# Kernel optimization log

Measured on AMD Instinct MI355X. Metric: run time of the kernel, lower is better.

## Reference

```python
import jax, jax.numpy as jnp
import numpy as np

N = 4096
D_IN = 1024
D_Q = 1024
D_V = 1024

def setup_inputs() -> dict:
    key = jax.random.key(0)
    ks = jax.random.split(key, 8)
    # x scaled down a bit so exp() of raw (unstable, no max-subtract) scores stays finite,
    # matching the original module's numerics regime.
    x = jax.random.normal(ks[0], (N, D_IN), dtype=jnp.float32) * 0.02
    mask = jax.random.uniform(ks[1], (N, N), dtype=jnp.float32)
    s = 1.0 / np.sqrt(D_IN)
    Wq = jax.random.normal(ks[2], (D_IN, D_Q), dtype=jnp.float32) * s
    bq = jax.random.normal(ks[3], (D_Q,), dtype=jnp.float32) * 0.02
    Wk = jax.random.normal(ks[4], (D_IN, D_Q), dtype=jnp.float32) * s
    bk = jax.random.normal(ks[5], (D_Q,), dtype=jnp.float32) * 0.02
    Wv = jax.random.normal(ks[6], (D_IN, D_V), dtype=jnp.float32) * s
    bv = jax.random.normal(ks[7], (D_V,), dtype=jnp.float32) * 0.02
    return {"x": x, "mask": mask, "Wq": Wq, "bq": bq, "Wk": Wk, "bk": bk, "Wv": Wv, "bv": bv}

def reference(x, mask, Wq, bq, Wk, bk, Wv, bv):
    # Q, K, V projections (nn.Linear: x @ W + b, here W stored as [in, out])
    Q = x @ Wq + bq          # [N, Dq]
    K = x @ Wk + bk          # [N, Dq]
    V = x @ Wv + bv          # [N, Dv]
    scale = 1.0              # default scale in original forward
    scores = scale * (Q @ K.T)   # [N, N]
    scores = mask * scores       # elementwise multiplicative mask
    # Faithful to original (quirky) normalization:
    # exp(S) / sum(exp(S), axis=1)[None, :]  -> row-sums broadcast across ROWS
    e = jnp.exp(scores)                       # [N, N]
    denom = jnp.sum(e, axis=1)[None, :]       # [1, N]
    softmax = e / denom                       # [N, N]
    return softmax @ V                        # [N, Dv]
```

## Files before the change

### kernel.cpp

```cpp
#include <hip/hip_runtime.h>
#include <hip/hip_bf16.h>


#define N_TOK 4096
#define D_DIM 1024
#define VS_SCALE 131072.0f

typedef __bf16 bf16x8 __attribute__((ext_vector_type(8)));
typedef __bf16 bf16x4 __attribute__((ext_vector_type(4)));
typedef float  f32x4  __attribute__((ext_vector_type(4)));

typedef const __attribute__((address_space(1))) char g_char;
typedef __attribute__((address_space(3))) char lds_char;

__device__ inline unsigned char f32_to_fp8(float f) {
    return (unsigned char)(__builtin_amdgcn_cvt_pk_fp8_f32(f, f, 0, false) & 0xff);
}

__global__ void cvt_and_bias(const float* __restrict__ x, __bf16* __restrict__ xb,
                             const float* __restrict__ bq, const float* __restrict__ bk,
                             const float* __restrict__ bv, float* __restrict__ bcat) {
    int b = blockIdx.x;
    if (b < 4096) {
        int i = (b * 256 + threadIdx.x) * 4;
        float4 v = *(const float4*)(x + i);
        bf16x4 o;
        o.x = (__bf16)v.x; o.y = (__bf16)v.y;
        o.z = (__bf16)v.z; o.w = (__bf16)v.w;
        *(bf16x4*)(xb + i) = o;
    } else {
        int i = (b - 4096) * 256 + threadIdx.x;
        if (i < 1024) bcat[i] = bq[i];
        else if (i < 2048) bcat[i] = bk[i - 1024];
        else if (i < 3072) bcat[i] = bv[i - 2048];
    }
}

__global__ void transpose_w3(const float* __restrict__ Wq, const float* __restrict__ Wk,
                             const float* __restrict__ Wv, __bf16* __restrict__ outT) {
    const float* in = (blockIdx.z == 0) ? Wq : (blockIdx.z == 1) ? Wk : Wv;
    __bf16* oT = outT + (size_t)blockIdx.z * 1024 * 1024;
    __shared__ float t[64][65];
    const int c0 = blockIdx.x * 64, r0 = blockIdx.y * 64;
    const int tid = threadIdx.x;
#pragma unroll
    for (int k = 0; k < 16; k++) {
        int lin = tid + k * 256;
        int r = lin >> 6, c = lin & 63;
        t[r][c] = in[(size_t)(r0 + r) * 1024 + c0 + c];
    }
    __syncthreads();
#pragma unroll
    for (int k = 0; k < 16; k++) {
        int lin = tid + k * 256;
        int c = lin >> 6, r = lin & 63;
        oT[(size_t)(c0 + c) * 1024 + r0 + r] = (__bf16)t[r][c];
    }
}

__global__ void scale_transpose(const __bf16* __restrict__ V, int ldv,
                                const float* __restrict__ denom,
                                unsigned char* __restrict__ VT8) {
    __shared__ float t[64][65];
    __shared__ float rd[64];
    const int d0 = blockIdx.x * 64, j0 = blockIdx.y * 64;
    const int tid = threadIdx.x;
    if (tid < 64) rd[tid] = VS_SCALE / denom[j0 + tid];
    __syncthreads();
#pragma unroll
    for (int k = 0; k < 16; k++) {
        int lin = tid + k * 256;
        int j = lin >> 6, d = lin & 63;
        t[j][d] = (float)V[(size_t)(j0 + j) * ldv + d0 + d] * rd[j];
    }
    __syncthreads();
#pragma unroll
    for (int k = 0; k < 16; k++) {
        int lin = tid + k * 256;
        int d = lin >> 6, j = lin & 63;
        VT8[(size_t)(d0 + d) * N_TOK + j0 + j] = f32_to_fp8(t[j][d]);
    }
}

template <int EPI>
__global__ __launch_bounds__(256, 2)
void gemm_nt(const __bf16* __restrict__ A, const __bf16* __restrict__ B,
             int lda, int ldb, int ldc, int K,
             const float* __restrict__ bias,
             const float* __restrict__ mask,
             __bf16* __restrict__ Cb, unsigned char* __restrict__ C8,
             float* __restrict__ denom) {
    __shared__ __bf16 lA[128 * 64];
    __shared__ __bf16 lB[128 * 64];

    const int tid  = threadIdx.x;
    const int wave = tid >> 6;
    const int lane = tid & 63;
    const int quad = lane >> 4;
    const int l16  = lane & 15;
    const int m0 = blockIdx.y * 128;
    const int n0 = blockIdx.x * 128;
    const int wr = (wave >> 1) * 64;
    const int wc = (wave & 1) * 64;

    const size_t lda_b = (size_t)lda * 2;
    const size_t ldb_b = (size_t)ldb * 2;
    const int tr = tid >> 3;
    const int ts = ((tid & 7) ^ (tr & 7)) * 16;
    const char* gA = (const char*)A + (size_t)(m0 + tr) * lda_b + ts;
    const char* gB = (const char*)B + (size_t)(n0 + tr) * ldb_b + ts;
    const size_t pstepA = (size_t)32 * lda_b;
    const size_t pstepB = (size_t)32 * ldb_b;

    lds_char* lAp = (lds_char*)(void*)lA + wave * 1024;
    lds_char* lBp = (lds_char*)(void*)lB + wave * 1024;

    const int l7 = l16 & 7;
    const int rdA0 = ((wr + l16) * 128 + ((quad ^ l7) * 16)) >> 1;
    const int rdA1 = ((wr + l16) * 128 + (((4 + quad) ^ l7) * 16)) >> 1;
    const int rdB0 = ((wc + l16) * 128 + ((quad ^ l7) * 16)) >> 1;
    const int rdB1 = ((wc + l16) * 128 + (((4 + quad) ^ l7) * 16)) >> 1;

    f32x4 acc[4][4];
#pragma unroll
    for (int i = 0; i < 4; i++)
#pragma unroll
        for (int j = 0; j < 4; j++) acc[i][j] = (f32x4){0.f, 0.f, 0.f, 0.f};

    for (int kt = 0; kt < K; kt += 64) {
#pragma unroll
        for (int c = 0; c < 4; c++)
            __builtin_amdgcn_global_load_lds((g_char*)(gA + c * pstepA),
                                             lAp + c * 4096, 16, 0, 0);
#pragma unroll
        for (int c = 0; c < 4; c++)
            __builtin_amdgcn_global_load_lds((g_char*)(gB + c * pstepB),
                                             lBp + c * 4096, 16, 0, 0);
        gA += 128;
        gB += 128;
        __syncthreads();

        bf16x8 af[4], bfr[4];
#pragma unroll
        for (int i = 0; i < 4; i++) af[i] = *(const bf16x8*)&lA[rdA0 + i * 1024];
#pragma unroll
        for (int j = 0; j < 4; j++) bfr[j] = *(const bf16x8*)&lB[rdB0 + j * 1024];
#pragma unroll
        for (int i = 0; i < 4; i++)
#pragma unroll
            for (int j = 0; j < 4; j++)
                acc[i][j] = __builtin_amdgcn_mfma_f32_16x16x32_bf16(
                    af[i], bfr[j], acc[i][j], 0, 0, 0);
#pragma unroll
        for (int i = 0; i < 4; i++) af[i] = *(const bf16x8*)&lA[rdA1 + i * 1024];
#pragma unroll
        for (int j = 0; j < 4; j++) bfr[j] = *(const bf16x8*)&lB[rdB1 + j * 1024];
#pragma unroll
        for (int i = 0; i < 4; i++)
#pragma unroll
            for (int j = 0; j < 4; j++)
                acc[i][j] = __builtin_amdgcn_mfma_f32_16x16x32_bf16(
                    af[i], bfr[j], acc[i][j], 0, 0, 0);
        __syncthreads();
    }

#pragma unroll
    for (int i = 0; i < 4; i++) {
        const int rbase = m0 + wr + i * 16 + quad * 4;
        f32x4 rs = (f32x4){0.f, 0.f, 0.f, 0.f};
#pragma unroll
        for (int j = 0; j < 4; j++) {
            const int col = n0 + wc + j * 16 + l16;
            f32x4 v = acc[i][j];
            if (EPI == 0) {
                const float bb = bias[col];
#pragma unroll
                for (int r = 0; r < 4; r++)
                    Cb[(size_t)(rbase + r) * ldc + col] = (__bf16)(v[r] + bb);
            } else {
#pragma unroll
                for (int r = 0; r < 4; r++) {
                    size_t idx = (size_t)(rbase + r) * ldc + col;
                    float e = __expf(mask[idx] * v[r]);
                    C8[idx] = f32_to_fp8(e);
                    rs[r] += e;
                }
            }
        }
        if (EPI == 1) {
#pragma unroll
            for (int m = 1; m < 16; m <<= 1) {
#pragma unroll
                for (int r = 0; r < 4; r++) rs[r] += __shfl_xor(rs[r], m, 64);
            }
            if (l16 == 0) {
#pragma unroll
                for (int r = 0; r < 4; r++) atomicAdd(&denom[rbase + r], rs[r]);
            }
        }
    }
}

__global__ __launch_bounds__(256, 2)
void gemm_out_fp8(const unsigned char* __restrict__ A,
                  const unsigned char* __restrict__ B,
                  float* __restrict__ C) {
    __shared__ unsigned char lA[128 * 128];
    __shared__ unsigned char lB[64 * 128];

    const int tid  = threadIdx.x;
    const int wave = tid >> 6;
    const int lane = tid & 63;
    const int quad = lane >> 4;
    const int l16  = lane & 15;
    const int m0 = blockIdx.y * 128;
    const int n0 = blockIdx.x * 64;
    const int wr = (wave >> 1) * 64;
    const int wc = (wave & 1) * 32;

    const int tr = tid >> 3;
    const int ts = ((tid & 7) ^ (tr & 7)) * 16;
    const char* gA = (const char*)A + (size_t)(m0 + tr) * N_TOK + ts;
    const char* gB = (const char*)B + (size_t)(n0 + tr) * N_TOK + ts;
    const size_t pstep = (size_t)32 * N_TOK;

    lds_char* lAp = (lds_char*)(void*)lA + wave * 1024;
    lds_char* lBp = (lds_char*)(void*)lB + wave * 1024;

    const int l7 = l16 & 7;
    const int qhi = quad >> 1, qlo = (quad & 1) * 8;
    int rdA[4], rdB[4];
#pragma unroll
    for (int k = 0; k < 4; k++) {
        rdA[k] = ((k * 2 + qhi) ^ l7) * 16 + qlo;
        rdB[k] = rdA[k];
    }

    f32x4 acc[4][2];
#pragma unroll
    for (int i = 0; i < 4; i++)
#pragma unroll
        for (int j = 0; j < 2; j++) acc[i][j] = (f32x4){0.f, 0.f, 0.f, 0.f};

    for (int kt = 0; kt < N_TOK; kt += 128) {
#pragma unroll
        for (int c = 0; c < 4; c++)
            __builtin_amdgcn_global_load_lds((g_char*)(gA + c * pstep),
                                             lAp + c * 4096, 16, 0, 0);
#pragma unroll
        for (int c = 0; c < 2; c++)
            __builtin_amdgcn_global_load_lds((g_char*)(gB + c * pstep),
                                             lBp + c * 4096, 16, 0, 0);
        gA += 128;
        gB += 128;
        __syncthreads();

#pragma unroll
        for (int k = 0; k < 4; k++) {
            long a[4], b[2];
#pragma unroll
            for (int i = 0; i < 4; i++)
                a[i] = *(const long*)&lA[(wr + i * 16 + l16) * 128 + rdA[k]];
#pragma unroll
            for (int j = 0; j < 2; j++)
                b[j] = *(const long*)&lB[(wc + j * 16 + l16) * 128 + rdB[k]];
#pragma unroll
            for (int i = 0; i < 4; i++)
#pragma unroll
                for (int j = 0; j < 2; j++)
                    acc[i][j] = __builtin_amdgcn_mfma_f32_16x16x32_fp8_fp8(
                        a[i], b[j], acc[i][j], 0, 0, 0);
        }
        __syncthreads();
    }

#pragma unroll
    for (int i = 0; i < 4; i++) {
#pragma unroll
        for (int j = 0; j < 2; j++) {
            const int col   = n0 + wc + j * 16 + l16;
            const int rbase = m0 + wr + i * 16 + quad * 4;
            f32x4 v = acc[i][j];
#pragma unroll
            for (int r = 0; r < 4; r++)
                C[(size_t)(rbase + r) * D_DIM + col] = v[r] * (1.0f / VS_SCALE);
        }
    }
}

extern "C" void kernel_launch(void* const* d_in, const int* in_sizes, int n_in,
                              void* d_out, int out_size, void* d_ws, size_t ws_size,
                              hipStream_t stream) {
    const float* x    = (const float*)d_in[0];
    const float* mask = (const float*)d_in[1];
    const float* Wq   = (const float*)d_in[2];
    const float* bq   = (const float*)d_in[3];
    const float* Wk   = (const float*)d_in[4];
    const float* bk   = (const float*)d_in[5];
    const float* Wv   = (const float*)d_in[6];
    const float* bv   = (const float*)d_in[7];
    float* out = (float*)d_out;
    char* ws = (char*)d_ws;

    const size_t MB = 1024 * 1024;
    unsigned char* E8   = (unsigned char*)(ws + 0 * MB);
    __bf16* QKVb  = (__bf16*)(ws + 16 * MB);
    __bf16* xb    = (__bf16*)(ws + 40 * MB);
    unsigned char* VsT8 = (unsigned char*)xb;
    __bf16* WcatT = (__bf16*)(ws + 48 * MB);
    float*  bcat  = (float*)(ws + 54 * MB);
    float*  denom = (float*)(ws + 54 * MB + 64 * 1024);

    hipMemsetAsync(denom, 0, N_TOK * sizeof(float), stream);

    cvt_and_bias<<<4096 + 12, 256, 0, stream>>>(x, xb, bq, bk, bv, bcat);
    transpose_w3<<<dim3(16, 16, 3), 256, 0, stream>>>(Wq, Wk, Wv, WcatT);

    gemm_nt<0><<<dim3(24, 32), 256, 0, stream>>>(
        xb, WcatT, D_DIM, D_DIM, 3 * D_DIM, D_DIM,
        bcat, nullptr, QKVb, nullptr, nullptr);

    const __bf16* Qb = QKVb;
    const __bf16* Kb = QKVb + D_DIM;
    gemm_nt<1><<<dim3(32, 32), 256, 0, stream>>>(
        Qb, Kb, 3 * D_DIM, 3 * D_DIM, N_TOK, D_DIM,
        nullptr, mask, nullptr, E8, denom);

    scale_transpose<<<dim3(16, 64), 256, 0, stream>>>(QKVb + 2048, 3 * D_DIM, denom, VsT8);

    gemm_out_fp8<<<dim3(16, 32), 256, 0, stream>>>(E8, VsT8, out);
}
```

Before: 245.4 us.

## Triple-buffer LDS tiles with async prefetch in both GEMM kernels

Both the bf16 NT GEMM and the fp8 output GEMM move from single-buffered LDS loads, with a full barrier each k-step, to a three-stage ring buffer. Tiles are prefetched two iterations ahead with global_load_lds, and partial vmcnt waits let each step wait only on its own tile. All LDS fragments for a step are loaded before the MFMAs, and s_setprio raises wave priority during the MFMA block. The goal is to hide global memory latency behind compute. The cost is three times the LDS per block, which may cut occupancy below two blocks per CU, especially for the bf16 kernel at 96KB.

```diff
diff --git a/kernel.cpp b/kernel.cpp
--- a/kernel.cpp
+++ b/kernel.cpp
@@ -90,8 +90,8 @@
              const float* __restrict__ mask,
              __bf16* __restrict__ Cb, unsigned char* __restrict__ C8,
              float* __restrict__ denom) {
-    __shared__ __bf16 lA[128 * 64];
-    __shared__ __bf16 lB[128 * 64];
+    __shared__ __bf16 lA[3 * 128 * 64];
+    __shared__ __bf16 lB[3 * 128 * 64];
 
     const int tid  = threadIdx.x;
     const int wave = tid >> 6;
@@ -112,8 +112,8 @@
     const size_t pstepA = (size_t)32 * lda_b;
     const size_t pstepB = (size_t)32 * ldb_b;
 
-    lds_char* lAp = (lds_char*)(void*)lA + wave * 1024;
-    lds_char* lBp = (lds_char*)(void*)lB + wave * 1024;
+    lds_char* lAs = (lds_char*)(void*)lA + wave * 1024;
+    lds_char* lBs = (lds_char*)(void*)lB + wave * 1024;
 
     const int l7 = l16 & 7;
     const int rdA0 = ((wr + l16) * 128 + ((quad ^ l7) * 16)) >> 1;
@@ -127,42 +127,69 @@
 #pragma unroll
         for (int j = 0; j < 4; j++) acc[i][j] = (f32x4){0.f, 0.f, 0.f, 0.f};
 
-    for (int kt = 0; kt < K; kt += 64) {
-#pragma unroll
-        for (int c = 0; c < 4; c++)
-            __builtin_amdgcn_global_load_lds((g_char*)(gA + c * pstepA),
-                                             lAp + c * 4096, 16, 0, 0);
-#pragma unroll
-        for (int c = 0; c < 4; c++)
-            __builtin_amdgcn_global_load_lds((g_char*)(gB + c * pstepB),
-                                             lBp + c * 4096, 16, 0, 0);
-        gA += 128;
-        gB += 128;
-        __syncthreads();
-
-        bf16x8 af[4], bfr[4];
-#pragma unroll
-        for (int i = 0; i < 4; i++) af[i] = *(const bf16x8*)&lA[rdA0 + i * 1024];
-#pragma unroll
-        for (int j = 0; j < 4; j++) bfr[j] = *(const bf16x8*)&lB[rdB0 + j * 1024];
+    const int NT = K >> 6;
+
+#define STAGE_NT(tt, bb) do {                                                         \
+    const char* ga_ = gA + (size_t)(tt) * 128;                                        \
+    const char* gb_ = gB + (size_t)(tt) * 128;                                        \
+    lds_char* la_ = lAs + (bb) * 16384;                                               \
+    lds_char* lb_ = lBs + (bb) * 16384;                                               \
+    __builtin_amdgcn_global_load_lds((g_char*)(ga_),              la_,         16, 0, 0); \
+    __builtin_amdgcn_global_load_lds((g_char*)(ga_ + pstepA),     la_ + 4096,  16, 0, 0); \
+    __builtin_amdgcn_global_load_lds((g_char*)(ga_ + 2 * pstepA), la_ + 8192,  16, 0, 0); \
+    __builtin_amdgcn_global_load_lds((g_char*)(ga_ + 3 * pstepA), la_ + 12288, 16, 0, 0); \
+    __builtin_amdgcn_global_load_lds((g_char*)(gb_),              lb_,         16, 0, 0); \
+    __builtin_amdgcn_global_load_lds((g_char*)(gb_ + pstepB),     lb_ + 4096,  16, 0, 0); \
+    __builtin_amdgcn_global_load_lds((g_char*)(gb_ + 2 * pstepB), lb_ + 8192,  16, 0, 0); \
+    __builtin_amdgcn_global_load_lds((g_char*)(gb_ + 3 * pstepB), lb_ + 12288, 16, 0, 0); \
+} while (0)
+
+    STAGE_NT(0, 0);
+    STAGE_NT(1, 1);
+    asm volatile("s_waitcnt vmcnt(8)" ::: "memory");
+    __builtin_amdgcn_s_barrier();
+    __builtin_amdgcn_sched_barrier(0);
+
+    for (int t = 0; t < NT; ++t) {
+        const int b = t % 3;
+        const bool pf = (t + 2 < NT);
+        if (pf) STAGE_NT(t + 2, (t + 2) % 3);
+
+        const __bf16* la = lA + b * 8192;
+        const __bf16* lb = lB + b * 8192;
+
+        bf16x8 a0[4], a1[4], bf0[4], bf1[4];
+#pragma unroll
+        for (int i = 0; i < 4; i++) {
+            a0[i] = *(const bf16x8*)&la[rdA0 + i * 1024];
+            a1[i] = *(const bf16x8*)&la[rdA1 + i * 1024];
+        }
+#pragma unroll
+        for (int j = 0; j < 4; j++) {
+            bf0[j] = *(const bf16x8*)&lb[rdB0 + j * 1024];
+            bf1[j] = *(const bf16x8*)&lb[rdB1 + j * 1024];
+        }
+        __builtin_amdgcn_s_setprio(1);
 #pragma unroll
         for (int i = 0; i < 4; i++)
 #pragma unroll
             for (int j = 0; j < 4; j++)
                 acc[i][j] = __builtin_amdgcn_mfma_f32_16x16x32_bf16(
-                    af[i], bfr[j], acc[i][j], 0, 0, 0);
-#pragma unroll
-        for (int i = 0; i < 4; i++) af[i] = *(const bf16x8*)&lA[rdA1 + i * 1024];
-#pragma unroll
-        for (int j = 0; j < 4; j++) bfr[j] = *(const bf16x8*)&lB[rdB1 + j * 1024];
+                    a0[i], bf0[j], acc[i][j], 0, 0, 0);
 #pragma unroll
         for (int i = 0; i < 4; i++)
 #pragma unroll
             for (int j = 0; j < 4; j++)
                 acc[i][j] = __builtin_amdgcn_mfma_f32_16x16x32_bf16(
-                    af[i], bfr[j], acc[i][j], 0, 0, 0);
-        __syncthreads();
-    }
+                    a1[i], bf1[j], acc[i][j], 0, 0, 0);
+        __builtin_amdgcn_s_setprio(0);
+        __builtin_amdgcn_sched_barrier(0);
+        if (pf) asm volatile("s_waitcnt vmcnt(8) lgkmcnt(0)" ::: "memory");
+        else    asm volatile("s_waitcnt vmcnt(0) lgkmcnt(0)" ::: "memory");
+        __builtin_amdgcn_s_barrier();
+        __builtin_amdgcn_sched_barrier(0);
+    }
+#undef STAGE_NT
 
 #pragma unroll
     for (int i = 0; i < 4; i++) {
@@ -205,8 +232,8 @@
 void gemm_out_fp8(const unsigned char* __restrict__ A,
                   const unsigned char* __restrict__ B,
                   float* __restrict__ C) {
-    __shared__ unsigned char lA[128 * 128];
-    __shared__ unsigned char lB[64 * 128];
+    __shared__ unsigned char lA[3 * 128 * 128];
+    __shared__ unsigned char lB[3 * 64 * 128];
 
     const int tid  = threadIdx.x;
     const int wave = tid >> 6;
@@ -224,8 +251,8 @@
     const char* gB = (const char*)B + (size_t)(n0 + tr) * N_TOK + ts;
     const size_t pstep = (size_t)32 * N_TOK;
 
-    lds_char* lAp = (lds_char*)(void*)lA + wave * 1024;
-    lds_char* lBp = (lds_char*)(void*)lB + wave * 1024;
+    lds_char* lAs = (lds_char*)(void*)lA + wave * 1024;
+    lds_char* lBs = (lds_char*)(void*)lB + wave * 1024;
 
     const int l7 = l16 & 7;
     const int qhi = quad >> 1, qlo = (quad & 1) * 8;
@@ -242,37 +269,62 @@
 #pragma unroll
         for (int j = 0; j < 2; j++) acc[i][j] = (f32x4){0.f, 0.f, 0.f, 0.f};
 
-    for (int kt = 0; kt < N_TOK; kt += 128) {
-#pragma unroll
-        for (int c = 0; c < 4; c++)
-            __builtin_amdgcn_global_load_lds((g_char*)(gA + c * pstep),
-                                             lAp + c * 4096, 16, 0, 0);
-#pragma unroll
-        for (int c = 0; c < 2; c++)
-            __builtin_amdgcn_global_load_lds((g_char*)(gB + c * pstep),
-                                             lBp + c * 4096, 16, 0, 0);
-        gA += 128;
-        gB += 128;
-        __syncthreads();
-
+    const int NT = N_TOK / 128;
+
+#define STAGE_O(tt, bb) do {                                                          \
+    const char* ga_ = gA + (size_t)(tt) * 128;                                        \
+    const char* gb_ = gB + (size_t)(tt) * 128;                                        \
+    lds_char* la_ = lAs + (bb) * 16384;                                               \
+    lds_char* lb_ = lBs + (bb) * 8192;                                                \
+    __builtin_amdgcn_global_load_lds((g_char*)(ga_),             la_,         16, 0, 0); \
+    __builtin_amdgcn_global_load_lds((g_char*)(ga_ + pstep),     la_ + 4096,  16, 0, 0); \
+    __builtin_amdgcn_global_load_lds((g_char*)(ga_ + 2 * pstep), la_ + 8192,  16, 0, 0); \
+    __builtin_amdgcn_global_load_lds((g_char*)(ga_ + 3 * pstep), la_ + 12288, 16, 0, 0); \
+    __builtin_amdgcn_global_load_lds((g_char*)(gb_),             lb_,         16, 0, 0); \
+    __builtin_amdgcn_global_load_lds((g_char*)(gb_ + pstep),     lb_ + 4096,  16, 0, 0); \
+} while (0)
+
+    STAGE_O(0, 0);
+    STAGE_O(1, 1);
+    asm volatile("s_waitcnt vmcnt(6)" ::: "memory");
+    __builtin_amdgcn_s_barrier();
+    __builtin_amdgcn_sched_barrier(0);
+
+    for (int t = 0; t < NT; ++t) {
+        const int b = t % 3;
+        const bool pf = (t + 2 < NT);
+        if (pf) STAGE_O(t + 2, (t + 2) % 3);
+
+        const unsigned char* la = lA + b * 16384;
+        const unsigned char* lb = lB + b * 8192;
+
+        long av[4][4], bv[4][2];
 #pragma unroll
         for (int k = 0; k < 4; k++) {
-            long a[4], b[2];
 #pragma unroll
             for (int i = 0; i < 4; i++)
-                a[i] = *(const long*)&lA[(wr + i * 16 + l16) * 128 + rdA[k]];
+                av[k][i] = *(const long*)&la[(wr + i * 16 + l16) * 128 + rdA[k]];
 #pragma unroll
             for (int j = 0; j < 2; j++)
-                b[j] = *(const long*)&lB[(wc + j * 16 + l16) * 128 + rdB[k]];
+                bv[k][j] = *(const long*)&lb[(wc + j * 16 + l16) * 128 + rdB[k]];
+        }
+        __builtin_amdgcn_s_setprio(1);
+#pragma unroll
+        for (int k = 0; k < 4; k++)
 #pragma unroll
             for (int i = 0; i < 4; i++)
 #pragma unroll
                 for (int j = 0; j < 2; j++)
                     acc[i][j] = __builtin_amdgcn_mfma_f32_16x16x32_fp8_fp8(
-                        a[i], b[j], acc[i][j], 0, 0, 0);
-        }
-        __syncthreads();
-    }
+                        av[k][i], bv[k][j], acc[i][j], 0, 0, 0);
+        __builtin_amdgcn_s_setprio(0);
+        __builtin_amdgcn_sched_barrier(0);
+        if (pf) asm volatile("s_waitcnt vmcnt(6) lgkmcnt(0)" ::: "memory");
+        else    asm volatile("s_waitcnt vmcnt(0) lgkmcnt(0)" ::: "memory");
+        __builtin_amdgcn_s_barrier();
+        __builtin_amdgcn_sched_barrier(0);
+    }
+#undef STAGE_O
 
 #pragma unroll
     for (int i = 0; i < 4; i++) {
```

Result: slower. 315.1 us (+28.4%).

## Use 256x256 double-buffered GEMM tiles with prefetch for QKV and scores

Applied to the files above, without the earlier changes.

Replaces the 128x128 single-buffered NT GEMM with a 512-thread, 256x256-tile kernel used for both the QKV projection and the scores GEMM. The k loop now double-buffers LDS and prefetches the next K slice through direct global-to-LDS loads, interleaved with the MFMA phases. It also adds explicit s_barrier, waitcnt, sched_barrier and setprio scheduling hints. The goal is more operand reuse per loaded byte and overlap of memory with compute. In exchange, the 128 KB of LDS per block limits residency to about one block per CU, and the QKV grid shrinks to 192 blocks, which may leave CUs idle.

```diff
diff --git a/kernel.cpp b/kernel.cpp
--- a/kernel.cpp
+++ b/kernel.cpp
@@ -83,25 +83,25 @@
 }
 
 template <int EPI>
-__global__ __launch_bounds__(256, 2)
-void gemm_nt(const __bf16* __restrict__ A, const __bf16* __restrict__ B,
-             int lda, int ldb, int ldc, int K,
-             const float* __restrict__ bias,
-             const float* __restrict__ mask,
-             __bf16* __restrict__ Cb, unsigned char* __restrict__ C8,
-             float* __restrict__ denom) {
-    __shared__ __bf16 lA[128 * 64];
-    __shared__ __bf16 lB[128 * 64];
+__global__ __launch_bounds__(512, 2)
+void gemm_nt_256(const __bf16* __restrict__ A, const __bf16* __restrict__ B,
+                 int lda, int ldb, int ldc, int K,
+                 const float* __restrict__ bias,
+                 const float* __restrict__ mask,
+                 __bf16* __restrict__ Cb, unsigned char* __restrict__ C8,
+                 float* __restrict__ denom) {
+    __shared__ __bf16 ldsb[2 * 32768];
 
     const int tid  = threadIdx.x;
     const int wave = tid >> 6;
     const int lane = tid & 63;
     const int quad = lane >> 4;
     const int l16  = lane & 15;
-    const int m0 = blockIdx.y * 128;
-    const int n0 = blockIdx.x * 128;
-    const int wr = (wave >> 1) * 64;
-    const int wc = (wave & 1) * 64;
+    const int l7   = l16 & 7;
+    const int m0 = blockIdx.y * 256;
+    const int n0 = blockIdx.x * 256;
+    const int wr = (wave >> 2) * 128;
+    const int wc = (wave & 3) * 64;
 
     const size_t lda_b = (size_t)lda * 2;
     const size_t ldb_b = (size_t)ldb * 2;
@@ -109,63 +109,86 @@
     const int ts = ((tid & 7) ^ (tr & 7)) * 16;
     const char* gA = (const char*)A + (size_t)(m0 + tr) * lda_b + ts;
     const char* gB = (const char*)B + (size_t)(n0 + tr) * ldb_b + ts;
-    const size_t pstepA = (size_t)32 * lda_b;
-    const size_t pstepB = (size_t)32 * ldb_b;
-
-    lds_char* lAp = (lds_char*)(void*)lA + wave * 1024;
-    lds_char* lBp = (lds_char*)(void*)lB + wave * 1024;
-
-    const int l7 = l16 & 7;
-    const int rdA0 = ((wr + l16) * 128 + ((quad ^ l7) * 16)) >> 1;
-    const int rdA1 = ((wr + l16) * 128 + (((4 + quad) ^ l7) * 16)) >> 1;
-    const int rdB0 = ((wc + l16) * 128 + ((quad ^ l7) * 16)) >> 1;
-    const int rdB1 = ((wc + l16) * 128 + (((4 + quad) ^ l7) * 16)) >> 1;
-
-    f32x4 acc[4][4];
-#pragma unroll
-    for (int i = 0; i < 4; i++)
+    const size_t rstepA = (size_t)64 * lda_b;
+    const size_t rstepB = (size_t)64 * ldb_b;
+
+    lds_char* lw = (lds_char*)(void*)ldsb + wave * 1024;
+
+    const int s0 = ((0 + quad) ^ l7) * 16;
+    const int s1 = ((4 + quad) ^ l7) * 16;
+    const int aRow = (wr + l16) * 128;
+    const int bRow = (wc + l16) * 128 + 32768;
+
+    f32x4 acc[8][4];
+#pragma unroll
+    for (int i = 0; i < 8; i++)
 #pragma unroll
         for (int j = 0; j < 4; j++) acc[i][j] = (f32x4){0.f, 0.f, 0.f, 0.f};
 
-    for (int kt = 0; kt < K; kt += 64) {
-#pragma unroll
-        for (int c = 0; c < 4; c++)
-            __builtin_amdgcn_global_load_lds((g_char*)(gA + c * pstepA),
-                                             lAp + c * 4096, 16, 0, 0);
-#pragma unroll
-        for (int c = 0; c < 4; c++)
-            __builtin_amdgcn_global_load_lds((g_char*)(gB + c * pstepB),
-                                             lBp + c * 4096, 16, 0, 0);
-        gA += 128;
-        gB += 128;
-        __syncthreads();
-
-        bf16x8 af[4], bfr[4];
-#pragma unroll
-        for (int i = 0; i < 4; i++) af[i] = *(const bf16x8*)&lA[rdA0 + i * 1024];
-#pragma unroll
-        for (int j = 0; j < 4; j++) bfr[j] = *(const bf16x8*)&lB[rdB0 + j * 1024];
-#pragma unroll
-        for (int i = 0; i < 4; i++)
-#pragma unroll
-            for (int j = 0; j < 4; j++)
-                acc[i][j] = __builtin_amdgcn_mfma_f32_16x16x32_bf16(
-                    af[i], bfr[j], acc[i][j], 0, 0, 0);
-#pragma unroll
-        for (int i = 0; i < 4; i++) af[i] = *(const bf16x8*)&lA[rdA1 + i * 1024];
-#pragma unroll
-        for (int j = 0; j < 4; j++) bfr[j] = *(const bf16x8*)&lB[rdB1 + j * 1024];
-#pragma unroll
-        for (int i = 0; i < 4; i++)
-#pragma unroll
-            for (int j = 0; j < 4; j++)
-                acc[i][j] = __builtin_amdgcn_mfma_f32_16x16x32_bf16(
-                    af[i], bfr[j], acc[i][j], 0, 0, 0);
-        __syncthreads();
-    }
-
-#pragma unroll
-    for (int i = 0; i < 4; i++) {
+    const int NT = K >> 6;
+
+#define STAGE4(tt, bb, gg) do {                                                       \
+    const char* ga_ = gA + (size_t)(tt) * 128 + (size_t)(2 * (gg)) * rstepA;          \
+    const char* gb_ = gB + (size_t)(tt) * 128 + (size_t)(2 * (gg)) * rstepB;          \
+    lds_char* la_ = lw + (bb) * 65536 + (2 * (gg)) * 8192;                            \
+    lds_char* lb_ = lw + (bb) * 65536 + 32768 + (2 * (gg)) * 8192;                    \
+    __builtin_amdgcn_global_load_lds((g_char*)(ga_),          la_,        16, 0, 0);  \
+    __builtin_amdgcn_global_load_lds((g_char*)(ga_ + rstepA), la_ + 8192, 16, 0, 0);  \
+    __builtin_amdgcn_global_load_lds((g_char*)(gb_),          lb_,        16, 0, 0);  \
+    __builtin_amdgcn_global_load_lds((g_char*)(gb_ + rstepB), lb_ + 8192, 16, 0, 0);  \
+} while (0)
+
+    STAGE4(0, 0, 0);
+    STAGE4(0, 0, 1);
+    asm volatile("s_waitcnt vmcnt(0)" ::: "memory");
+    __builtin_amdgcn_s_barrier();
+
+    for (int t = 0; t < NT; ++t) {
+        const int cb = t & 1;
+        const char* buf = (const char*)ldsb + cb * 65536;
+        const bool pf = (t + 1 < NT);
+        bf16x8 bfr[4][2];
+
+#pragma unroll
+        for (int p = 0; p < 4; p++) {
+            if (p == 0) {
+#pragma unroll
+                for (int j = 0; j < 4; j++) {
+                    bfr[j][0] = *(const bf16x8*)(buf + bRow + j * 2048 + s0);
+                    bfr[j][1] = *(const bf16x8*)(buf + bRow + j * 2048 + s1);
+                }
+            }
+            bf16x8 aF[2][2];
+#pragma unroll
+            for (int ii = 0; ii < 2; ii++) {
+                aF[ii][0] = *(const bf16x8*)(buf + aRow + (2 * p + ii) * 2048 + s0);
+                aF[ii][1] = *(const bf16x8*)(buf + aRow + (2 * p + ii) * 2048 + s1);
+            }
+            if (p < 2 && pf) STAGE4(t + 1, cb ^ 1, p);
+
+            __builtin_amdgcn_s_barrier();
+            asm volatile("s_waitcnt lgkmcnt(0)" ::: "memory");
+            __builtin_amdgcn_sched_barrier(0);
+            __builtin_amdgcn_s_setprio(1);
+#pragma unroll
+            for (int ii = 0; ii < 2; ii++)
+#pragma unroll
+                for (int j = 0; j < 4; j++) {
+                    acc[2 * p + ii][j] = __builtin_amdgcn_mfma_f32_16x16x32_bf16(
+                        aF[ii][0], bfr[j][0], acc[2 * p + ii][j], 0, 0, 0);
+                    acc[2 * p + ii][j] = __builtin_amdgcn_mfma_f32_16x16x32_bf16(
+                        aF[ii][1], bfr[j][1], acc[2 * p + ii][j], 0, 0, 0);
+                }
+            __builtin_amdgcn_s_setprio(0);
+            __builtin_amdgcn_sched_barrier(0);
+            if (p == 3) asm volatile("s_waitcnt vmcnt(0)" ::: "memory");
+            __builtin_amdgcn_s_barrier();
+        }
+    }
+#undef STAGE4
+
+#pragma unroll
+    for (int i = 0; i < 8; i++) {
         const int rbase = m0 + wr + i * 16 + quad * 4;
         f32x4 rs = (f32x4){0.f, 0.f, 0.f, 0.f};
 #pragma unroll
@@ -316,13 +339,13 @@
     cvt_and_bias<<<4096 + 12, 256, 0, stream>>>(x, xb, bq, bk, bv, bcat);
     transpose_w3<<<dim3(16, 16, 3), 256, 0, stream>>>(Wq, Wk, Wv, WcatT);
 
-    gemm_nt<0><<<dim3(24, 32), 256, 0, stream>>>(
+    gemm_nt_256<0><<<dim3(12, 16), 512, 0, stream>>>(
         xb, WcatT, D_DIM, D_DIM, 3 * D_DIM, D_DIM,
         bcat, nullptr, QKVb, nullptr, nullptr);
 
     const __bf16* Qb = QKVb;
     const __bf16* Kb = QKVb + D_DIM;
-    gemm_nt<1><<<dim3(32, 32), 256, 0, stream>>>(
+    gemm_nt_256<1><<<dim3(16, 16), 512, 0, stream>>>(
         Qb, Kb, 3 * D_DIM, 3 * D_DIM, N_TOK, D_DIM,
         nullptr, mask, nullptr, E8, denom);
 
```

Result: slower. 252.2 us (+2.8%).
